# Optimization experiments

Hardware: AMD Instinct MI355X
Metric: run time of the kernel (lower is better)

The kernel has to match this reference:

```python
import jax, jax.numpy as jnp
import numpy as np

BITWIDTH = 7
M, K, N = 32768, 1024, 1024  # tokens, in_features, out_features


def _clip8(x):
    return jnp.clip(x, -127, 127).astype(jnp.int8)


def _range_bits(x):
    # RangeEstimate: ceil(log2(max|x|)) as int, 0 if all-zero
    r = jnp.max(jnp.abs(x).astype(jnp.float32))
    bits = jnp.ceil(jnp.log2(jnp.maximum(r, 1.0)))
    return jnp.where(r == 0, 0, bits).astype(jnp.int32)


def _round_shift(x, shift):
    # RoundShift (stochastic-style bit-shift rounding); shift is a traced int32 >= 1
    p = jnp.left_shift(jnp.int32(1), shift)
    rt = jnp.floor_divide(x, p)
    prob = x - rt * p
    dec = jnp.floor_divide(prob, jnp.left_shift(jnp.int32(1), shift - 1))
    return _clip8(rt + dec)


def setup_inputs() -> dict:
    key = jax.random.key(0)
    k1, k2 = jax.random.split(key)
    act_in = jax.random.randint(k1, (M, K), -127, 128, dtype=jnp.int32).astype(jnp.int8)
    weight = jax.random.randint(k2, (N, K), -127, 128, dtype=jnp.int32).astype(jnp.int8)
    exp_in = jnp.int32(0)
    weight_exp = jnp.int32(-11)  # ceil(log2(xavier bound)) - 7 for 1024x1024
    return {"act_in": act_in, "weight": weight, "exp_in": exp_in, "weight_exp": weight_exp}


def reference(act_in, weight, exp_in, weight_exp):
    # int8 GEMM with int32 accumulation: [M,K] @ [K,N]
    acc = jnp.matmul(act_in.astype(jnp.int32), weight.T.astype(jnp.int32))
    # act_calc: range-estimate + conditional bit-shift requantize to int8
    bits = _range_bits(acc)
    shift = bits - BITWIDTH
    pos = shift > 0
    sc = jnp.maximum(shift, 1)  # safe shift for the untaken branch
    act_out = jnp.where(pos, _round_shift(acc, sc), acc.astype(jnp.int8))
    exp_out = jnp.where(pos, exp_in + weight_exp + shift, exp_in + weight_exp)
    return act_out, exp_out
```

## Files before the change

kernel.cpp:

```cpp
#include <hip/hip_runtime.h>
#include <stdint.h>


#define MM 32768
#define NN 1024
#define KK 1024
#define BM 128
#define BN 128
#define BK 128
#define NKT (KK / BK)

typedef __attribute__((ext_vector_type(4))) int i32x4;
typedef __attribute__((ext_vector_type(16))) int i32x16;

__device__ __forceinline__ int pack4(int a, int b, int c, int d) {
  return (int)((unsigned)(a & 0xff) | ((unsigned)(b & 0xff) << 8) |
               ((unsigned)(c & 0xff) << 16) | ((unsigned)(d & 0xff) << 24));
}

__global__ void k_init(unsigned* slot) {
  if (threadIdx.x == 0) *slot = 0u;
}

__global__ void k_pack(const int* __restrict__ src, int8_t* __restrict__ dst, int n) {
  long t = (long)blockIdx.x * blockDim.x + threadIdx.x;
  long stride = (long)gridDim.x * blockDim.x;
  for (long i = t * 16; i < (long)n; i += stride * 16) {
    const i32x4* s = (const i32x4*)(src + i);
    i32x4 a0 = s[0], a1 = s[1], a2 = s[2], a3 = s[3];
    i32x4 o;
    o[0] = pack4(a0[0], a0[1], a0[2], a0[3]);
    o[1] = pack4(a1[0], a1[1], a1[2], a1[3]);
    o[2] = pack4(a2[0], a2[1], a2[2], a2[3]);
    o[3] = pack4(a3[0], a3[1], a3[2], a3[3]);
    *(i32x4*)(dst + i) = o;
  }
}

template <bool PACKED>
__global__ __launch_bounds__(256, 2)
void k_gemm(const void* __restrict__ Ap, const void* __restrict__ Bp,
            int* __restrict__ out, unsigned* __restrict__ maxslot) {
  __shared__ int8_t As[2][BM * BK];
  __shared__ int8_t Bs[2][BN * BK];

  const int tid  = threadIdx.x;
  const int lane = tid & 63;
  const int w    = tid >> 6;
  const int wr   = w >> 1;
  const int wc   = w & 1;

  const int orig = blockIdx.x;
  const int wgid = ((orig & 7) << 8) + (orig >> 3);
  const int bn = wgid & (NN / BN - 1);
  const int bm = wgid >> 3;
  const int m0 = bm * BM;
  const int n0 = bn * BN;

  i32x16 acc[2][2];
#pragma unroll
  for (int i = 0; i < 2; ++i)
#pragma unroll
    for (int j = 0; j < 2; ++j) acc[i][j] = 0;

  auto stage = [&](int buf, int kt) {
    const int k0 = kt * BK;
    if constexpr (PACKED) {
      const int8_t* A8 = (const int8_t*)Ap;
      const int8_t* B8 = (const int8_t*)Bp;
#pragma unroll
      for (int q = 0; q < 4; ++q) {
        const int p   = (w * 4 + q) * 1024 + lane * 16;
        const int row = p >> 7;
        const int col = (p & 127) ^ ((row & 7) << 4);
        __builtin_amdgcn_global_load_lds(
            (const __attribute__((address_space(1))) void*)(A8 + (size_t)(m0 + row) * KK + k0 + col),
            (__attribute__((address_space(3))) void*)(&As[buf][(w * 4 + q) * 1024]),
            16, 0, 0);
        __builtin_amdgcn_global_load_lds(
            (const __attribute__((address_space(1))) void*)(B8 + (size_t)(n0 + row) * KK + k0 + col),
            (__attribute__((address_space(3))) void*)(&Bs[buf][(w * 4 + q) * 1024]),
            16, 0, 0);
      }
    } else {
      const int* A32 = (const int*)Ap;
      const int* B32 = (const int*)Bp;
#pragma unroll
      for (int q = 0; q < 4; ++q) {
        const int p   = (w * 4 + q) * 1024 + lane * 16;
        const int row = p >> 7;
        const int col = (p & 127) ^ ((row & 7) << 4);
        const int* sa = A32 + (size_t)(m0 + row) * KK + k0 + col;
        const int* sb = B32 + (size_t)(n0 + row) * KK + k0 + col;
        i32x4 av, bv;
#pragma unroll
        for (int t = 0; t < 4; ++t) {
          i32x4 ta = ((const i32x4*)sa)[t];
          i32x4 tb = ((const i32x4*)sb)[t];
          av[t] = pack4(ta[0], ta[1], ta[2], ta[3]);
          bv[t] = pack4(tb[0], tb[1], tb[2], tb[3]);
        }
        *(i32x4*)(&As[buf][p]) = av;
        *(i32x4*)(&Bs[buf][p]) = bv;
      }
    }
  };

  auto compute = [&](int buf) {
#pragma unroll
    for (int ks = 0; ks < 4; ++ks) {
      i32x4 af[2], bf[2];
#pragma unroll
      for (int mi = 0; mi < 2; ++mi) {
        const int row = wr * 64 + mi * 32 + (lane & 31);
        int a = row * BK + ks * 32 + ((lane >> 5) << 4);
        a ^= (row & 7) << 4;
        af[mi] = *(const i32x4*)(&As[buf][a]);
      }
#pragma unroll
      for (int ni = 0; ni < 2; ++ni) {
        const int row = wc * 64 + ni * 32 + (lane & 31);
        int a = row * BK + ks * 32 + ((lane >> 5) << 4);
        a ^= (row & 7) << 4;
        bf[ni] = *(const i32x4*)(&Bs[buf][a]);
      }
#pragma unroll
      for (int mi = 0; mi < 2; ++mi)
#pragma unroll
        for (int ni = 0; ni < 2; ++ni)
          acc[mi][ni] = __builtin_amdgcn_mfma_i32_32x32x32_i8(
              af[mi], bf[ni], acc[mi][ni], 0, 0, 0);
    }
  };

  stage(0, 0);
  __syncthreads();
  for (int kt = 0; kt < NKT; ++kt) {
    if (kt + 1 < NKT) stage((kt + 1) & 1, kt + 1);
    compute(kt & 1);
    __syncthreads();
  }

  int mx = 0;
#pragma unroll
  for (int mi = 0; mi < 2; ++mi)
#pragma unroll
    for (int ni = 0; ni < 2; ++ni)
#pragma unroll
      for (int rg = 0; rg < 16; ++rg) {
        int x = acc[mi][ni][rg];
        int a = x < 0 ? -x : x;
        mx = a > mx ? a : mx;
      }
#pragma unroll
  for (int off = 32; off >= 1; off >>= 1) {
    int o = __shfl_xor(mx, off);
    mx = o > mx ? o : mx;
  }
  if (lane == 0) atomicMax(maxslot, (unsigned)mx);

#pragma unroll
  for (int mi = 0; mi < 2; ++mi)
#pragma unroll
    for (int ni = 0; ni < 2; ++ni) {
      const int mbase = m0 + wr * 64 + mi * 32;
      const int ncol  = n0 + wc * 64 + ni * 32 + (lane & 31);
#pragma unroll
      for (int rg = 0; rg < 16; ++rg) {
        const int mrow = mbase + (rg & 3) + ((rg >> 2) << 3) + ((lane >> 5) << 2);
        out[(size_t)mrow * NN + ncol] = acc[mi][ni][rg];
      }
    }
}

__global__ __launch_bounds__(256)
void k_requant(int* __restrict__ out, const unsigned* __restrict__ maxslot) {
  const unsigned r = *maxslot;
  const int bits  = (r <= 1u) ? 0 : (32 - __clz((int)(r - 1u)));
  const int shift = bits - 7;
  const size_t n = (size_t)MM * NN;
  size_t i = ((size_t)blockIdx.x * blockDim.x + threadIdx.x) * 4;
  const size_t stride = (size_t)gridDim.x * blockDim.x * 4;
  if (shift > 0) {
    for (; i < n; i += stride) {
      i32x4 v = *(i32x4*)(out + i);
#pragma unroll
      for (int j = 0; j < 4; ++j) {
        const int x = v[j];
        int t = (x >> shift) + ((x >> (shift - 1)) & 1);
        v[j] = t > 127 ? 127 : (t < -127 ? -127 : t);
      }
      *(i32x4*)(out + i) = v;
    }
  } else {
    for (; i < n; i += stride) {
      i32x4 v = *(i32x4*)(out + i);
#pragma unroll
      for (int j = 0; j < 4; ++j) v[j] = (int)(int8_t)v[j];
      *(i32x4*)(out + i) = v;
    }
  }
}

__global__ void k_final(int* __restrict__ out, const int* __restrict__ exp_in,
                        const int* __restrict__ wexp) {
  if (threadIdx.x == 0) {
    const unsigned r = *(const unsigned*)(out + (size_t)MM * NN);
    const int bits  = (r <= 1u) ? 0 : (32 - __clz((int)(r - 1u)));
    const int shift = bits - 7;
    out[(size_t)MM * NN] = *exp_in + *wexp + (shift > 0 ? shift : 0);
  }
}

extern "C" void kernel_launch(void* const* d_in, const int* in_sizes, int n_in,
                              void* d_out, int out_size, void* d_ws, size_t ws_size,
                              hipStream_t stream) {
  const int* act    = (const int*)d_in[0];
  const int* wgt    = (const int*)d_in[1];
  const int* exp_in = (const int*)d_in[2];
  const int* wexp   = (const int*)d_in[3];
  int* out          = (int*)d_out;
  unsigned* maxslot = (unsigned*)(out + (size_t)MM * NN);

  const size_t need = (size_t)(MM + NN) * KK + 256;
  const int gemm_grid = (MM / BM) * (NN / BN);

  k_init<<<1, 64, 0, stream>>>(maxslot);

  if (ws_size >= need) {
    int8_t* a8 = (int8_t*)d_ws;
    int8_t* w8 = a8 + (size_t)MM * KK;
    k_pack<<<2048, 256, 0, stream>>>(act, a8, MM * KK);
    k_pack<<<256, 256, 0, stream>>>(wgt, w8, NN * KK);
    k_gemm<true><<<gemm_grid, 256, 0, stream>>>(a8, w8, out, maxslot);
  } else {
    k_gemm<false><<<gemm_grid, 256, 0, stream>>>(act, wgt, out, maxslot);
  }

  k_requant<<<4096, 256, 0, stream>>>(out, maxslot);
  k_final<<<1, 64, 0, stream>>>(out, exp_in, wexp);
}
```

Baseline: 198.7 us.

## Use 256x128 tiles, 8 waves and a triple-buffered LDS pipeline in int8 GEMM

The packed GEMM path now uses 256-row tiles with 512 threads (8 waves) and a three-stage LDS ring. Loads are issued two k-tiles ahead, with explicit vmcnt waits, split barriers and s_setprio raised around the MFMA bursts. The goal is to overlap global-to-LDS traffic with matrix work and reuse B over more rows. The unpacked fallback is moved into a separate, simpler single-buffered kernel. LDS per block triples to 144KB, which may limit the block to one per CU despite the launch bound of 2.

```diff
diff --git a/kernel.cpp b/kernel.cpp
--- a/kernel.cpp
+++ b/kernel.cpp
@@ -5,10 +5,12 @@
 #define MM 32768
 #define NN 1024
 #define KK 1024
-#define BM 128
+#define BM 256
 #define BN 128
 #define BK 128
 #define NKT (KK / BK)
+#define TILE_A (BM * BK)
+#define TILE_B (BN * BK)
 
 typedef __attribute__((ext_vector_type(4))) int i32x4;
 typedef __attribute__((ext_vector_type(16))) int i32x16;
@@ -37,22 +39,21 @@
   }
 }
 
-template <bool PACKED>
-__global__ __launch_bounds__(256, 2)
-void k_gemm(const void* __restrict__ Ap, const void* __restrict__ Bp,
+__global__ __launch_bounds__(512, 2)
+void k_gemm(const int8_t* __restrict__ A8, const int8_t* __restrict__ B8,
             int* __restrict__ out, unsigned* __restrict__ maxslot) {
-  __shared__ int8_t As[2][BM * BK];
-  __shared__ int8_t Bs[2][BN * BK];
+  __shared__ int8_t As[3][TILE_A];
+  __shared__ int8_t Bs[3][TILE_B];
 
   const int tid  = threadIdx.x;
   const int lane = tid & 63;
   const int w    = tid >> 6;
-  const int wr   = w >> 1;
-  const int wc   = w & 1;
+  const int wm   = w >> 1;
+  const int wn   = w & 1;
 
   const int orig = blockIdx.x;
-  const int wgid = ((orig & 7) << 8) + (orig >> 3);
-  const int bn = wgid & (NN / BN - 1);
+  const int wgid = ((orig & 7) << 7) + (orig >> 3);
+  const int bn = wgid & 7;
   const int bm = wgid >> 3;
   const int m0 = bm * BM;
   const int n0 = bn * BN;
@@ -63,82 +64,76 @@
 #pragma unroll
     for (int j = 0; j < 2; ++j) acc[i][j] = 0;
 
-  auto stage = [&](int buf, int kt) {
-    const int k0 = kt * BK;
-    if constexpr (PACKED) {
-      const int8_t* A8 = (const int8_t*)Ap;
-      const int8_t* B8 = (const int8_t*)Bp;
-#pragma unroll
-      for (int q = 0; q < 4; ++q) {
-        const int p   = (w * 4 + q) * 1024 + lane * 16;
-        const int row = p >> 7;
-        const int col = (p & 127) ^ ((row & 7) << 4);
-        __builtin_amdgcn_global_load_lds(
-            (const __attribute__((address_space(1))) void*)(A8 + (size_t)(m0 + row) * KK + k0 + col),
-            (__attribute__((address_space(3))) void*)(&As[buf][(w * 4 + q) * 1024]),
-            16, 0, 0);
-        __builtin_amdgcn_global_load_lds(
-            (const __attribute__((address_space(1))) void*)(B8 + (size_t)(n0 + row) * KK + k0 + col),
-            (__attribute__((address_space(3))) void*)(&Bs[buf][(w * 4 + q) * 1024]),
-            16, 0, 0);
-      }
-    } else {
-      const int* A32 = (const int*)Ap;
-      const int* B32 = (const int*)Bp;
-#pragma unroll
-      for (int q = 0; q < 4; ++q) {
-        const int p   = (w * 4 + q) * 1024 + lane * 16;
-        const int row = p >> 7;
-        const int col = (p & 127) ^ ((row & 7) << 4);
-        const int* sa = A32 + (size_t)(m0 + row) * KK + k0 + col;
-        const int* sb = B32 + (size_t)(n0 + row) * KK + k0 + col;
-        i32x4 av, bv;
-#pragma unroll
-        for (int t = 0; t < 4; ++t) {
-          i32x4 ta = ((const i32x4*)sa)[t];
-          i32x4 tb = ((const i32x4*)sb)[t];
-          av[t] = pack4(ta[0], ta[1], ta[2], ta[3]);
-          bv[t] = pack4(tb[0], tb[1], tb[2], tb[3]);
+  auto stageA = [&](int buf, int kt, int L) {
+    const int p   = w * 4096 + L * 1024 + lane * 16;
+    const int row = p >> 7;
+    const int col = (p & 127) ^ ((row & 7) << 4);
+    __builtin_amdgcn_global_load_lds(
+        (const __attribute__((address_space(1))) void*)(A8 + (size_t)(m0 + row) * KK + kt * BK + col),
+        (__attribute__((address_space(3))) void*)(&As[buf][w * 4096 + L * 1024]),
+        16, 0, 0);
+  };
+  auto stageB = [&](int buf, int kt, int L) {
+    const int p   = w * 2048 + L * 1024 + lane * 16;
+    const int row = p >> 7;
+    const int col = (p & 127) ^ ((row & 7) << 4);
+    __builtin_amdgcn_global_load_lds(
+        (const __attribute__((address_space(1))) void*)(B8 + (size_t)(n0 + row) * KK + kt * BK + col),
+        (__attribute__((address_space(3))) void*)(&Bs[buf][w * 2048 + L * 1024]),
+        16, 0, 0);
+  };
+
+  stageA(0, 0, 0); stageA(0, 0, 1); stageA(0, 0, 2); stageA(0, 0, 3);
+  stageB(0, 0, 0); stageB(0, 0, 1);
+  stageA(1, 1, 0); stageA(1, 1, 1); stageA(1, 1, 2); stageA(1, 1, 3);
+  stageB(1, 1, 0); stageB(1, 1, 1);
+  asm volatile("s_waitcnt vmcnt(6)" ::: "memory");
+  __builtin_amdgcn_sched_barrier(0);
+  __builtin_amdgcn_s_barrier();
+
+  int cur = 0;
+  for (int kt = 0; kt < NKT; ++kt) {
+    int nxt = cur + 2; if (nxt >= 3) nxt -= 3;
+    const bool more = (kt + 2 < NKT);
+#pragma unroll
+    for (int q = 0; q < 2; ++q) {
+      if (more) {
+        if (q == 0) { stageA(nxt, kt + 2, 0); stageA(nxt, kt + 2, 1); stageB(nxt, kt + 2, 0); }
+        else        { stageA(nxt, kt + 2, 2); stageA(nxt, kt + 2, 3); stageB(nxt, kt + 2, 1); }
+      }
+      i32x4 af[2][4], bf[4];
+#pragma unroll
+      for (int ks = 0; ks < 4; ++ks) {
+        const int brow = wn * 64 + q * 32 + (lane & 31);
+        const int ba = brow * BK + ((ks * 32 + ((lane >> 5) << 4)) ^ ((brow & 7) << 4));
+        bf[ks] = *(const i32x4*)(&Bs[cur][ba]);
+      }
+#pragma unroll
+      for (int mi = 0; mi < 2; ++mi)
+#pragma unroll
+        for (int ks = 0; ks < 4; ++ks) {
+          const int arow = wm * 64 + mi * 32 + (lane & 31);
+          const int aa = arow * BK + ((ks * 32 + ((lane >> 5) << 4)) ^ ((arow & 7) << 4));
+          af[mi][ks] = *(const i32x4*)(&As[cur][aa]);
         }
-        *(i32x4*)(&As[buf][p]) = av;
-        *(i32x4*)(&Bs[buf][p]) = bv;
-      }
-    }
-  };
-
-  auto compute = [&](int buf) {
-#pragma unroll
-    for (int ks = 0; ks < 4; ++ks) {
-      i32x4 af[2], bf[2];
-#pragma unroll
-      for (int mi = 0; mi < 2; ++mi) {
-        const int row = wr * 64 + mi * 32 + (lane & 31);
-        int a = row * BK + ks * 32 + ((lane >> 5) << 4);
-        a ^= (row & 7) << 4;
-        af[mi] = *(const i32x4*)(&As[buf][a]);
-      }
-#pragma unroll
-      for (int ni = 0; ni < 2; ++ni) {
-        const int row = wc * 64 + ni * 32 + (lane & 31);
-        int a = row * BK + ks * 32 + ((lane >> 5) << 4);
-        a ^= (row & 7) << 4;
-        bf[ni] = *(const i32x4*)(&Bs[buf][a]);
-      }
-#pragma unroll
-      for (int mi = 0; mi < 2; ++mi)
-#pragma unroll
-        for (int ni = 0; ni < 2; ++ni)
-          acc[mi][ni] = __builtin_amdgcn_mfma_i32_32x32x32_i8(
-              af[mi], bf[ni], acc[mi][ni], 0, 0, 0);
-    }
-  };
-
-  stage(0, 0);
-  __syncthreads();
-  for (int kt = 0; kt < NKT; ++kt) {
-    if (kt + 1 < NKT) stage((kt + 1) & 1, kt + 1);
-    compute(kt & 1);
-    __syncthreads();
+      __builtin_amdgcn_sched_barrier(0);
+      __builtin_amdgcn_s_barrier();
+      __builtin_amdgcn_s_setprio(1);
+#pragma unroll
+      for (int ks = 0; ks < 4; ++ks)
+#pragma unroll
+        for (int mi = 0; mi < 2; ++mi)
+          acc[mi][q] = __builtin_amdgcn_mfma_i32_32x32x32_i8(
+              af[mi][ks], bf[ks], acc[mi][q], 0, 0, 0);
+      __builtin_amdgcn_s_setprio(0);
+      if (q == 1) {
+        if (more)                 { asm volatile("s_waitcnt vmcnt(6)" ::: "memory"); }
+        else if (kt + 1 < NKT)    { asm volatile("s_waitcnt vmcnt(0)" ::: "memory"); }
+      }
+      __builtin_amdgcn_sched_barrier(0);
+      __builtin_amdgcn_s_barrier();
+    }
+    cur = cur + 1 == 3 ? 0 : cur + 1;
   }
 
   int mx = 0;
@@ -163,8 +158,101 @@
   for (int mi = 0; mi < 2; ++mi)
 #pragma unroll
     for (int ni = 0; ni < 2; ++ni) {
+      const int mbase = m0 + wm * 64 + mi * 32;
+      const int ncol  = n0 + wn * 64 + ni * 32 + (lane & 31);
+#pragma unroll
+      for (int rg = 0; rg < 16; ++rg) {
+        const int mrow = mbase + (rg & 3) + ((rg >> 2) << 3) + ((lane >> 5) << 2);
+        out[(size_t)mrow * NN + ncol] = acc[mi][ni][rg];
+      }
+    }
+}
+
+__global__ __launch_bounds__(256, 2)
+void k_gemm_fb(const int* __restrict__ A32, const int* __restrict__ B32,
+               int* __restrict__ out, unsigned* __restrict__ maxslot) {
+  __shared__ int8_t As[128 * 128];
+  __shared__ int8_t Bs[128 * 128];
+  const int tid = threadIdx.x, lane = tid & 63, w = tid >> 6;
+  const int wr = w >> 1, wc = w & 1;
+  const int bn = blockIdx.x & 7, bm = blockIdx.x >> 3;
+  const int m0 = bm * 128, n0 = bn * 128;
+  i32x16 acc[2][2];
+#pragma unroll
+  for (int i = 0; i < 2; ++i)
+#pragma unroll
+    for (int j = 0; j < 2; ++j) acc[i][j] = 0;
+  for (int kt = 0; kt < 8; ++kt) {
+    const int k0 = kt * 128;
+    __syncthreads();
+#pragma unroll
+    for (int j = 0; j < 4; ++j) {
+      const int fb = (j * 256 + tid) * 16;
+      const int row = fb >> 7;
+      const int swz = fb ^ ((row & 7) << 4);
+      const int col = fb & 127;
+      const int* sa = A32 + (size_t)(m0 + row) * KK + k0 + col;
+      const int* sb = B32 + (size_t)(n0 + row) * KK + k0 + col;
+      i32x4 av, bv;
+#pragma unroll
+      for (int t = 0; t < 4; ++t) {
+        i32x4 ta = ((const i32x4*)sa)[t];
+        i32x4 tb = ((const i32x4*)sb)[t];
+        av[t] = pack4(ta[0], ta[1], ta[2], ta[3]);
+        bv[t] = pack4(tb[0], tb[1], tb[2], tb[3]);
+      }
+      *(i32x4*)(As + swz) = av;
+      *(i32x4*)(Bs + swz) = bv;
+    }
+    __syncthreads();
+#pragma unroll
+    for (int ks = 0; ks < 4; ++ks) {
+      i32x4 af[2], bf[2];
+#pragma unroll
+      for (int mi = 0; mi < 2; ++mi) {
+        const int row = wr * 64 + mi * 32 + (lane & 31);
+        int a = row * 128 + ks * 32 + ((lane >> 5) << 4);
+        a ^= (row & 7) << 4;
+        af[mi] = *(const i32x4*)(As + a);
+      }
+#pragma unroll
+      for (int ni = 0; ni < 2; ++ni) {
+        const int row = wc * 64 + ni * 32 + (lane & 31);
+        int a = row * 128 + ks * 32 + ((lane >> 5) << 4);
+        a ^= (row & 7) << 4;
+        bf[ni] = *(const i32x4*)(Bs + a);
+      }
+#pragma unroll
+      for (int mi = 0; mi < 2; ++mi)
+#pragma unroll
+        for (int ni = 0; ni < 2; ++ni)
+          acc[mi][ni] = __builtin_amdgcn_mfma_i32_32x32x32_i8(
+              af[mi], bf[ni], acc[mi][ni], 0, 0, 0);
+    }
+  }
+  int mx = 0;
+#pragma unroll
+  for (int mi = 0; mi < 2; ++mi)
+#pragma unroll
+    for (int ni = 0; ni < 2; ++ni)
+#pragma unroll
+      for (int rg = 0; rg < 16; ++rg) {
+        int x = acc[mi][ni][rg];
+        int a = x < 0 ? -x : x;
+        mx = a > mx ? a : mx;
+      }
+#pragma unroll
+  for (int off = 32; off >= 1; off >>= 1) {
+    int o = __shfl_xor(mx, off);
+    mx = o > mx ? o : mx;
+  }
+  if (lane == 0) atomicMax(maxslot, (unsigned)mx);
+#pragma unroll
+  for (int mi = 0; mi < 2; ++mi)
+#pragma unroll
+    for (int ni = 0; ni < 2; ++ni) {
       const int mbase = m0 + wr * 64 + mi * 32;
-      const int ncol  = n0 + wc * 64 + ni * 32 + (lane & 31);
+      const int ncol = n0 + wc * 64 + ni * 32 + (lane & 31);
 #pragma unroll
       for (int rg = 0; rg < 16; ++rg) {
         const int mrow = mbase + (rg & 3) + ((rg >> 2) << 3) + ((lane >> 5) << 2);
@@ -223,7 +311,6 @@
   unsigned* maxslot = (unsigned*)(out + (size_t)MM * NN);
 
   const size_t need = (size_t)(MM + NN) * KK + 256;
-  const int gemm_grid = (MM / BM) * (NN / BN);
 
   k_init<<<1, 64, 0, stream>>>(maxslot);
 
@@ -232,9 +319,10 @@
     int8_t* w8 = a8 + (size_t)MM * KK;
     k_pack<<<2048, 256, 0, stream>>>(act, a8, MM * KK);
     k_pack<<<256, 256, 0, stream>>>(wgt, w8, NN * KK);
-    k_gemm<true><<<gemm_grid, 256, 0, stream>>>(a8, w8, out, maxslot);
+    const int grid = (MM / BM) * (NN / BN);
+    k_gemm<<<grid, 512, 0, stream>>>(a8, w8, out, maxslot);
   } else {
-    k_gemm<false><<<gemm_grid, 256, 0, stream>>>(act, wgt, out, maxslot);
+    k_gemm_fb<<<(MM / 128) * (NN / 128), 256, 0, stream>>>(act, wgt, out, maxslot);
   }
 
   k_requant<<<4096, 256, 0, stream>>>(out, maxslot);
```

After: 211.9 us. +6.7%, slower.
